# Kernel optimization log

Measured on AMD Instinct MI355X. Metric: run time of the kernel, lower is better.

Reference implementation:

```python
import jax, jax.numpy as jnp
import numpy as np

NUM_ITERATIONS = 3
B, M, P, D, O, I = 32, 32, 196, 20, 16, 8


def squash(s, axis=-1):
    # v = (||s||^2 / (1+||s||^2)) * s/||s||
    sq = jnp.sum(s * s, axis=axis, keepdims=True)
    return (sq / (1.0 + sq)) * s / jnp.sqrt(sq + 1e-9)


def setup_inputs() -> dict:
    key = jax.random.key(0)
    kx, kw = jax.random.split(key)
    x = jax.random.normal(kx, (B, M, P, I), dtype=jnp.float32)
    W = jax.random.normal(kw, (1, M, P, D, O, I), dtype=jnp.float32)
    return {"x": x, "W": W}


def reference(x, W):
    b_, m, p, i = x.shape
    Wm = W[0]  # [M,P,D,O,I]
    # u_hat = W @ u : batched matvec -> [B,M,P,D,O]
    u_hat = jnp.einsum('mpdoi,bmpi->bmpdo', Wm, x)
    d = u_hat.shape[3]
    b = jnp.zeros((b_, m, p, d), dtype=x.dtype)
    c = None
    v = None
    for it in range(NUM_ITERATIONS):
        # softmax jointly over (num_in_caps * num_digit_cap), matching view+softmax(dim=2)
        c = jax.nn.softmax(b.reshape(b_, m, p * d), axis=2).reshape(b_, m, p, d)
        # s = sum over maps and in-caps of c * u_hat -> [B,D,O]
        s = jnp.einsum('bmpd,bmpdo->bdo', c, u_hat)
        v = squash(s, axis=-1)
        if it != NUM_ITERATIONS - 1:
            # agreement: u_hat^T v -> [B,M,P,D]
            b = b + jnp.einsum('bmpdo,bdo->bmpd', u_hat, v)
    map_size = int(np.sqrt(p))
    weighted = c[..., None] * u_hat  # [B,M,P,D,O]
    xm = weighted.reshape(b_, m, map_size, map_size, d, -1)
    c_maps = jnp.sqrt(jnp.sum(xm * xm, axis=-1))  # [B,M,ms,ms,D]
    features = jnp.mean(weighted, axis=2)  # [B,M,D,O]
    return v, c_maps, features
```

## Files before the change

### kernel.cpp

```cpp
#include <hip/hip_runtime.h>
#include <math.h>

#define B_   32
#define M_   32
#define P_   196
#define D_   20
#define O_   16
#define I_   8
#define DO_  320
#define PD_  3920
#define ROW_ 62720

#define CMAPS_OFF 10240
#define FEAT_OFF  4024320

#define UH_FLOATS 16056320

__device__ __forceinline__ unsigned short f2bf(float v) {
    unsigned int u = __float_as_uint(v);
    return (unsigned short)((u + 0x7fffu + ((u >> 16) & 1u)) >> 16);
}
__device__ __forceinline__ float bfhi(unsigned int w) { return __uint_as_float(w & 0xffff0000u); }
__device__ __forceinline__ float bflo(unsigned int w) { return __uint_as_float(w << 16); }

__global__ __launch_bounds__(256)
void caps_u(const float* __restrict__ x, const float* __restrict__ W,
            unsigned short* __restrict__ uh)
{
    __shared__ float x_lds[7 * 260];
    const int m  = blockIdx.x / 28;
    const int pt = blockIdx.x % 28;
    const int p0 = pt * 7;
    const int t  = threadIdx.x;
    const int bq = t >> 5, doq = t & 31;

    for (int f = t; f < 7 * 32 * 2; f += 256) {
        int b = f / 14, r = f % 14, p = r >> 1, h = r & 1;
        *(float4*)(x_lds + p * 260 + b * 8 + h * 4) =
            *(const float4*)(x + (((size_t)b * M_ + m) * P_ + p0 + p) * I_ + h * 4);
    }
    __syncthreads();

    for (int pl = 0; pl < 7; pl++) {
        const float* wp = W + (size_t)(m * P_ + p0 + pl) * DO_ * I_;
        float xr[4][8];
        #pragma unroll
        for (int bb = 0; bb < 4; bb++) {
            float4 a0 = *(const float4*)(x_lds + pl * 260 + (bq * 4 + bb) * 8);
            float4 a1 = *(const float4*)(x_lds + pl * 260 + (bq * 4 + bb) * 8 + 4);
            xr[bb][0]=a0.x; xr[bb][1]=a0.y; xr[bb][2]=a0.z; xr[bb][3]=a0.w;
            xr[bb][4]=a1.x; xr[bb][5]=a1.y; xr[bb][6]=a1.z; xr[bb][7]=a1.w;
        }
        unsigned short* uhp[4];
        #pragma unroll
        for (int bb = 0; bb < 4; bb++)
            uhp[bb] = uh + (((size_t)(bq * 4 + bb) * M_ + m) * P_ + p0 + pl) * DO_ + doq;
        #pragma unroll
        for (int j = 0; j < 10; j++) {
            const float4* w4 = (const float4*)(wp + (doq + 32 * j) * I_);
            float4 w0 = w4[0], w1 = w4[1];
            #pragma unroll
            for (int bb = 0; bb < 4; bb++) {
                float s = w0.x * xr[bb][0];
                s = fmaf(w0.y, xr[bb][1], s);
                s = fmaf(w0.z, xr[bb][2], s);
                s = fmaf(w0.w, xr[bb][3], s);
                s = fmaf(w1.x, xr[bb][4], s);
                s = fmaf(w1.y, xr[bb][5], s);
                s = fmaf(w1.z, xr[bb][6], s);
                s = fmaf(w1.w, xr[bb][7], s);
                uhp[bb][32 * j] = f2bf(s);
            }
        }
    }
}

template<int MODE>
__global__ __launch_bounds__(320)
void route_k(const unsigned short* __restrict__ uh, const float* __restrict__ vin,
             float* __restrict__ pbm, float* __restrict__ out)
{
    extern __shared__ float sm[];
    float* accL  = sm;
    float* red   = sm + 320 * 17;
    float* blogL = red + 16;
    float* usqL  = blogL + 3920;

    const int blk = blockIdx.x;
    const int t = threadIdx.x;
    const int d = t % 20;
    const int k = t / 20;
    const int pstart = k * 12 + (k < 4 ? k : 4);
    const int pcnt   = (k < 4) ? 13 : 12;
    const unsigned short* up = uh + (size_t)blk * ROW_;

    float vreg[16];
    if (MODE) {
        const float* vb = vin + (size_t)(blk >> 5) * DO_;
        #pragma unroll
        for (int o = 0; o < 16; o++) vreg[o] = vb[d * 16 + o];
    }
    float acc[16];
    #pragma unroll
    for (int o = 0; o < 16; o++) acc[o] = 0.f;
    float mloc = -1e30f, Z = 0.f;

    for (int pp = 0; pp < pcnt; pp++) {
        const int p = pstart + pp;
        const float4* a = (const float4*)(up + (size_t)p * DO_ + d * 16);
        float4 a0 = a[0], a1 = a[1];
        unsigned int ua[8];
        ua[0]=__float_as_uint(a0.x); ua[1]=__float_as_uint(a0.y);
        ua[2]=__float_as_uint(a0.z); ua[3]=__float_as_uint(a0.w);
        ua[4]=__float_as_uint(a1.x); ua[5]=__float_as_uint(a1.y);
        ua[6]=__float_as_uint(a1.z); ua[7]=__float_as_uint(a1.w);
        float u[16];
        #pragma unroll
        for (int q = 0; q < 8; q++) { u[2*q] = bflo(ua[q]); u[2*q+1] = bfhi(ua[q]); }

        if (MODE) {
            float bl = u[0] * vreg[0];
            #pragma unroll
            for (int o = 1; o < 16; o++) bl = fmaf(u[o], vreg[o], bl);
            if (MODE == 2) {
                float us = u[0] * u[0];
                #pragma unroll
                for (int o = 1; o < 16; o++) us = fmaf(u[o], u[o], us);
                blogL[p * D_ + d] = bl;
                usqL[p * D_ + d]  = us;
            }
            if (bl > mloc + 8.f) {
                float r = __expf(mloc - bl);
                Z *= r;
                #pragma unroll
                for (int o = 0; o < 16; o++) acc[o] *= r;
                mloc = bl;
            }
            float e = __expf(bl - mloc);
            Z += e;
            #pragma unroll
            for (int o = 0; o < 16; o++) acc[o] = fmaf(e, u[o], acc[o]);
        } else {
            #pragma unroll
            for (int o = 0; o < 16; o++) acc[o] += u[o];
        }
    }

    float f = 1.f, iz = 1.f, mx = 0.f;
    if (MODE) {
        mx = mloc;
        #pragma unroll
        for (int msk = 1; msk < 64; msk <<= 1) mx = fmaxf(mx, __shfl_xor(mx, msk, 64));
        if ((t & 63) == 0) red[t >> 6] = mx;
        __syncthreads();
        mx = fmaxf(fmaxf(fmaxf(red[0], red[1]), fmaxf(red[2], red[3])), red[4]);
        f = __expf(mloc - mx);
        float zz = Z * f;
        #pragma unroll
        for (int msk = 1; msk < 64; msk <<= 1) zz += __shfl_xor(zz, msk, 64);
        if ((t & 63) == 0) red[8 + (t >> 6)] = zz;
        __syncthreads();
        iz = 1.f / (red[8] + red[9] + red[10] + red[11] + red[12]);
    }
    #pragma unroll
    for (int o = 0; o < 16; o++) accL[t * 17 + o] = acc[o] * f;
    __syncthreads();
    {
        const int dd = t >> 4, oo = t & 15;
        float s = 0.f;
        #pragma unroll
        for (int kk = 0; kk < 16; kk++) s += accL[(kk * 20 + dd) * 17 + oo];
        s *= iz;
        pbm[(size_t)blk * DO_ + t] = s;
        if (MODE == 2) out[FEAT_OFF + (size_t)blk * DO_ + t] = s * (1.f / 196.f);
    }
    if (MODE == 2) {
        for (int e = t; e < PD_; e += 320)
            out[CMAPS_OFF + (size_t)blk * PD_ + e] =
                __expf(blogL[e] - mx) * iz * sqrtf(usqL[e]);
    }
}

template<int WH>
__global__ __launch_bounds__(320)
void sq2_k(const float* __restrict__ pbm, float* __restrict__ v1,
           float* __restrict__ vs, float* __restrict__ out)
{
    const int b = blockIdx.x, t = threadIdx.x;
    float s = 0.f;
    for (int mi = 0; mi < M_; mi++) s += pbm[((size_t)b * M_ + mi) * DO_ + t];
    if (WH == 0) s *= (1.f / PD_);
    float sq = s * s;
    #pragma unroll
    for (int msk = 1; msk < 16; msk <<= 1) sq += __shfl_xor(sq, msk, 16);
    float vr = (sq / (1.f + sq)) * s * rsqrtf(sq + 1e-9f);
    if (WH == 0) v1[(size_t)b * DO_ + t] = vr;
    if (WH == 1) vs[(size_t)b * DO_ + t] = v1[(size_t)b * DO_ + t] + vr;
    if (WH == 2) out[(size_t)b * DO_ + t] = vr;
}

extern "C" void kernel_launch(void* const* d_in, const int* in_sizes, int n_in,
                              void* d_out, int out_size, void* d_ws, size_t ws_size,
                              hipStream_t stream)
{
    const float* x = (const float*)d_in[0];
    const float* W = (const float*)d_in[1];
    float* out = (float*)d_out;

    unsigned short* uh = (unsigned short*)d_ws;
    float* fws = (float*)((char*)d_ws + (size_t)64225280 * 2);
    float* pbm = fws;
    float* v1  = pbm + (size_t)B_ * M_ * DO_;
    float* vs  = v1 + (size_t)B_ * DO_;

    const size_t LDS_A = (320 * 17 + 16) * sizeof(float);
    const size_t LDS_B = LDS_A + 2 * PD_ * sizeof(float);

    caps_u<<<M_ * 28, 256, 0, stream>>>(x, W, uh);

    route_k<0><<<B_ * M_, 320, LDS_A, stream>>>(uh, v1, pbm, out);
    sq2_k<0><<<B_, 320, 0, stream>>>(pbm, v1, vs, out);

    route_k<1><<<B_ * M_, 320, LDS_A, stream>>>(uh, v1, pbm, out);
    sq2_k<1><<<B_, 320, 0, stream>>>(pbm, v1, vs, out);

    route_k<2><<<B_ * M_, 320, LDS_B, stream>>>(uh, vs, pbm, out);
    sq2_k<2><<<B_, 320, 0, stream>>>(pbm, v1, vs, out);
}
```

Baseline: 121.5 us.

## Restructure u_hat kernel for 16-byte packed bf16 stores and per-thread W rows

The u_hat kernel is remapped so each thread owns 8 consecutive (d,o) outputs for 4 batches. It loads 64 W floats into registers and writes the results as one packed 16-byte bf16 store, replacing the scattered 2-byte stores. The block grows to 320 threads and each block now covers 4 positions instead of 7, giving more blocks. This aims to cut write transactions on the large u_hat tensor, at the cost of higher register pressure from the 64-float W array.

```diff
diff --git a/kernel.cpp b/kernel.cpp
--- a/kernel.cpp
+++ b/kernel.cpp
@@ -14,63 +14,62 @@
 #define CMAPS_OFF 10240
 #define FEAT_OFF  4024320
 
-#define UH_FLOATS 16056320
-
 __device__ __forceinline__ unsigned short f2bf(float v) {
     unsigned int u = __float_as_uint(v);
     return (unsigned short)((u + 0x7fffu + ((u >> 16) & 1u)) >> 16);
 }
+__device__ __forceinline__ unsigned int pk2(float lo, float hi) {
+    return (unsigned int)f2bf(lo) | ((unsigned int)f2bf(hi) << 16);
+}
 __device__ __forceinline__ float bfhi(unsigned int w) { return __uint_as_float(w & 0xffff0000u); }
 __device__ __forceinline__ float bflo(unsigned int w) { return __uint_as_float(w << 16); }
 
-__global__ __launch_bounds__(256)
+#define PT4  4
+#define NPT4 49
+__global__ __launch_bounds__(320)
 void caps_u(const float* __restrict__ x, const float* __restrict__ W,
             unsigned short* __restrict__ uh)
 {
-    __shared__ float x_lds[7 * 260];
-    const int m  = blockIdx.x / 28;
-    const int pt = blockIdx.x % 28;
-    const int p0 = pt * 7;
+    __shared__ float x_lds[PT4 * 260];
+    const int m  = blockIdx.x / NPT4;
+    const int pt = blockIdx.x % NPT4;
+    const int p0 = pt * PT4;
     const int t  = threadIdx.x;
-    const int bq = t >> 5, doq = t & 31;
-
-    for (int f = t; f < 7 * 32 * 2; f += 256) {
-        int b = f / 14, r = f % 14, p = r >> 1, h = r & 1;
+    const int g  = t % 40;
+    const int bq = t / 40;
+
+    if (t < 256) {
+        int p = t >> 6, b = (t >> 1) & 31, h = t & 1;
         *(float4*)(x_lds + p * 260 + b * 8 + h * 4) =
             *(const float4*)(x + (((size_t)b * M_ + m) * P_ + p0 + p) * I_ + h * 4);
     }
     __syncthreads();
 
-    for (int pl = 0; pl < 7; pl++) {
-        const float* wp = W + (size_t)(m * P_ + p0 + pl) * DO_ * I_;
-        float xr[4][8];
+    #pragma unroll 1
+    for (int pl = 0; pl < PT4; pl++) {
+        const float* wp = W + ((size_t)(m * P_ + p0 + pl) * DO_ + g * 8) * I_;
+        float w[64];
+        #pragma unroll
+        for (int q = 0; q < 16; q++)
+            *(float4*)(w + q * 4) = *(const float4*)(wp + q * 4);
         #pragma unroll
         for (int bb = 0; bb < 4; bb++) {
-            float4 a0 = *(const float4*)(x_lds + pl * 260 + (bq * 4 + bb) * 8);
-            float4 a1 = *(const float4*)(x_lds + pl * 260 + (bq * 4 + bb) * 8 + 4);
-            xr[bb][0]=a0.x; xr[bb][1]=a0.y; xr[bb][2]=a0.z; xr[bb][3]=a0.w;
-            xr[bb][4]=a1.x; xr[bb][5]=a1.y; xr[bb][6]=a1.z; xr[bb][7]=a1.w;
-        }
-        unsigned short* uhp[4];
-        #pragma unroll
-        for (int bb = 0; bb < 4; bb++)
-            uhp[bb] = uh + (((size_t)(bq * 4 + bb) * M_ + m) * P_ + p0 + pl) * DO_ + doq;
-        #pragma unroll
-        for (int j = 0; j < 10; j++) {
-            const float4* w4 = (const float4*)(wp + (doq + 32 * j) * I_);
-            float4 w0 = w4[0], w1 = w4[1];
-            #pragma unroll
-            for (int bb = 0; bb < 4; bb++) {
-                float s = w0.x * xr[bb][0];
-                s = fmaf(w0.y, xr[bb][1], s);
-                s = fmaf(w0.z, xr[bb][2], s);
-                s = fmaf(w0.w, xr[bb][3], s);
-                s = fmaf(w1.x, xr[bb][4], s);
-                s = fmaf(w1.y, xr[bb][5], s);
-                s = fmaf(w1.z, xr[bb][6], s);
-                s = fmaf(w1.w, xr[bb][7], s);
-                uhp[bb][32 * j] = f2bf(s);
+            const int b = bq * 4 + bb;
+            float xr[8];
+            *(float4*)(xr)     = *(const float4*)(x_lds + pl * 260 + b * 8);
+            *(float4*)(xr + 4) = *(const float4*)(x_lds + pl * 260 + b * 8 + 4);
+            float u[8];
+            #pragma unroll
+            for (int r = 0; r < 8; r++) {
+                float s = w[r * 8] * xr[0];
+                #pragma unroll
+                for (int i = 1; i < 8; i++) s = fmaf(w[r * 8 + i], xr[i], s);
+                u[r] = s;
             }
+            uint4 pkv;
+            pkv.x = pk2(u[0], u[1]); pkv.y = pk2(u[2], u[3]);
+            pkv.z = pk2(u[4], u[5]); pkv.w = pk2(u[6], u[7]);
+            *(uint4*)(uh + (((size_t)b * M_ + m) * P_ + p0 + pl) * DO_ + g * 8) = pkv;
         }
     }
 }
@@ -216,7 +215,7 @@
     const size_t LDS_A = (320 * 17 + 16) * sizeof(float);
     const size_t LDS_B = LDS_A + 2 * PD_ * sizeof(float);
 
-    caps_u<<<M_ * 28, 256, 0, stream>>>(x, W, uh);
+    caps_u<<<M_ * NPT4, 320, 0, stream>>>(x, W, uh);
 
     route_k<0><<<B_ * M_, 320, LDS_A, stream>>>(uh, v1, pbm, out);
     sq2_k<0><<<B_, 320, 0, stream>>>(pbm, v1, vs, out);
```

Result: slower. 161.7 us (+33.1%).
